# Kernel optimization log

Hardware: AMD Instinct MI355X
Metric: run time of the kernel (lower is better)

Reference implementation:

```python
import jax, jax.numpy as jnp
import numpy as np

V, E, C, H = 32000, 512, 512, 1024
B, S = 8, 512
EPS = 1e-5


def _ln(x, g, b):
    m = jnp.mean(x, axis=-1, keepdims=True)
    v = jnp.var(x, axis=-1, keepdims=True)
    return (x - m) * jax.lax.rsqrt(v + EPS) * g + b


def setup_inputs() -> dict:
    key = jax.random.key(0)
    ks = jax.random.split(key, 12)
    std = 0.02
    return {
        "input_ids": jax.random.randint(ks[0], (B, S), 0, V, dtype=jnp.int32),
        "emb": jax.random.normal(ks[1], (V, E), jnp.float32) * std,
        "emb_g": jnp.ones((E,), jnp.float32),
        "emb_b": jnp.zeros((E,), jnp.float32),
        "W1": jax.random.normal(ks[2], (E + C, H), jnp.float32) * std,
        "b1": jnp.zeros((H,), jnp.float32),
        "W2": jax.random.normal(ks[3], (H, H), jnp.float32) * std,
        "b2": jnp.zeros((H,), jnp.float32),
        "Wout": jax.random.normal(ks[4], (H, V), jnp.float32) * std,
        "bout": jnp.zeros((V,), jnp.float32),
        "Wg": jax.random.normal(ks[5], (H + C, C), jnp.float32) * std,
        "bg": jnp.zeros((C,), jnp.float32),
        "Wc": jax.random.normal(ks[6], (H + C, C), jnp.float32) * std,
        "bc": jnp.zeros((C,), jnp.float32),
        "cn_g": jnp.ones((C,), jnp.float32),
        "cn_b": jnp.zeros((C,), jnp.float32),
    }


def reference(input_ids, emb, emb_g, emb_b, W1, b1, W2, b2, Wout, bout,
              Wg, bg, Wc, bc, cn_g, cn_b):
    # token embedding + norm: [B,S,E]
    tok = _ln(emb[input_ids], emb_g, emb_b)
    tok_t = jnp.swapaxes(tok, 0, 1)  # [S,B,E] for scan over time

    def step(context, x_t):
        # context: [B,C], x_t: [B,E]
        fnn_in = jnp.concatenate([x_t, context], axis=-1)          # [B,E+C]
        h1 = jax.nn.relu(fnn_in @ W1 + b1)                          # [B,H]
        h2 = jax.nn.relu(h1 @ W2 + b2)                              # [B,H]
        logits_t = h2 @ Wout + bout                                 # [B,V]
        comb = jnp.concatenate([h2, context], axis=-1)              # [B,H+C]
        gate = jax.nn.sigmoid(comb @ Wg + bg)
        cand = jnp.tanh(comb @ Wc + bc)
        new_ctx = gate * cand + (1.0 - gate) * context
        new_ctx = jnp.clip(_ln(new_ctx, cn_g, cn_b), -10.0, 10.0)
        return new_ctx, (logits_t, new_ctx)

    ctx0 = jnp.zeros((input_ids.shape[0], C), jnp.float32)
    _, (logits, traj) = jax.lax.scan(step, ctx0, tok_t)
    logits = jnp.swapaxes(logits, 0, 1)  # [B,S,V]
    traj = jnp.swapaxes(traj, 0, 1)      # [B,S,C]
    return logits, traj
```

## Files before the change

kernel.cpp:

```cpp
#include <hip/hip_runtime.h>

typedef unsigned short u16;
typedef unsigned int u32;
typedef unsigned long long u64;
typedef __attribute__((ext_vector_type(8))) short bf16x8;
typedef __attribute__((ext_vector_type(4))) float f32x4;

#define SMEM_SCAN 147968

__device__ __forceinline__ u16 f2bf(float f) {
  u32 u = __float_as_uint(f);
  u += 0x7fffu + ((u >> 16) & 1u);
  return (u16)(u >> 16);
}

__device__ __forceinline__ void async16(const void* g, void* l) {
  __builtin_amdgcn_global_load_lds((const __attribute__((address_space(1))) void*)g,
                                   (__attribute__((address_space(3))) void*)l, 16, 0, 0);
}

__device__ __forceinline__ void st_f32(float* p, float v) {
  __hip_atomic_store(p, v, __ATOMIC_RELAXED, __HIP_MEMORY_SCOPE_AGENT);
}
__device__ __forceinline__ void st_u16(u16* p, u16 v) {
  __hip_atomic_store(p, v, __ATOMIC_RELAXED, __HIP_MEMORY_SCOPE_AGENT);
}
__device__ __forceinline__ void st_f32x2(float* p, float a, float b) {
  u64 v = ((u64)__float_as_uint(b) << 32) | (u64)__float_as_uint(a);
  __hip_atomic_store((u64*)p, v, __ATOMIC_RELAXED, __HIP_MEMORY_SCOPE_AGENT);
}
__device__ __forceinline__ u32 ld_u32(const u32* p) {
  return __hip_atomic_load(p, __ATOMIC_RELAXED, __HIP_MEMORY_SCOPE_AGENT);
}

__device__ __forceinline__ void gridbar(u32* bar, u32 target, int wg) {
  __syncthreads();
  const int tid = threadIdx.x;
  if (wg == 0) {
    if (tid < 64) {
      const u32* a0 = bar + tid;
      const u32* a1 = bar + 64 + tid;
      for (;;) {
        u32 v0 = ld_u32(a0);
        u32 v1 = ld_u32(a1);
        bool ok = ((v0 >= target) | (tid == 0)) & (v1 >= target);
        if (__all(ok)) break;
        __builtin_amdgcn_s_sleep(2);
      }
      if (tid == 0)
        __hip_atomic_store(bar + 160, target, __ATOMIC_RELAXED, __HIP_MEMORY_SCOPE_AGENT);
    }
  } else if (tid == 0) {
    __hip_atomic_store(bar + wg, target, __ATOMIC_RELAXED, __HIP_MEMORY_SCOPE_AGENT);
    while (ld_u32(bar + 160) < target)
      __builtin_amdgcn_s_sleep(2);
  }
  if (tid == 0) __builtin_amdgcn_fence(__ATOMIC_ACQUIRE, "agent");
  __syncthreads();
}

__global__ void __launch_bounds__(256)
k_embed_f32(const int* __restrict__ ids, const float* __restrict__ emb,
            const float* __restrict__ g, const float* __restrict__ b, float* __restrict__ tok) {
  int r = blockIdx.x;
  int s = r >> 3, bch = r & 7;
  int id = ids[bch * 512 + s];
  const float* row = emb + (size_t)id * 512;
  int tid = threadIdx.x;
  float2 v = *(const float2*)&row[tid * 2];
  float sum = v.x + v.y, sq = v.x * v.x + v.y * v.y;
  #pragma unroll
  for (int o = 1; o < 64; o <<= 1) { sum += __shfl_xor(sum, o); sq += __shfl_xor(sq, o); }
  __shared__ float rs[4][2];
  int w = tid >> 6;
  if ((tid & 63) == 0) { rs[w][0] = sum; rs[w][1] = sq; }
  __syncthreads();
  float S = rs[0][0] + rs[1][0] + rs[2][0] + rs[3][0];
  float Q = rs[0][1] + rs[1][1] + rs[2][1] + rs[3][1];
  float m = S * (1.f / 512.f);
  float rstd = rsqrtf(Q * (1.f / 512.f) - m * m + 1e-5f);
  int e = tid * 2;
  float2 o2;
  o2.x = (v.x - m) * rstd * g[e] + b[e];
  o2.y = (v.y - m) * rstd * g[e + 1] + b[e + 1];
  *(float2*)&tok[(size_t)r * 512 + e] = o2;
}

__global__ void __launch_bounds__(256)
k_transpose(const float* __restrict__ src, u16* __restrict__ dst,
            int K, int N, int stride) {
  __shared__ float tl[64][65];
  int k0 = blockIdx.x << 6, n0 = blockIdx.y << 6;
  int tid = threadIdx.x;
  int a = tid >> 6, c = tid & 63;
  #pragma unroll
  for (int p = 0; p < 64; p += 4)
    tl[p + a][c] = src[(size_t)(k0 + p + a) * stride + n0 + c];
  __syncthreads();
  #pragma unroll
  for (int p = 0; p < 64; p += 4)
    dst[(size_t)(n0 + p + a) * K + k0 + c] = f2bf(tl[c][p + a]);
}

__global__ void __launch_bounds__(256)
k_transpose_f32(const float* __restrict__ src, float* __restrict__ dst,
                int K, int N, int stride) {
  __shared__ float tl[64][65];
  int k0 = blockIdx.x << 6, n0 = blockIdx.y << 6;
  int tid = threadIdx.x;
  int a = tid >> 6, c = tid & 63;
  #pragma unroll
  for (int p = 0; p < 64; p += 4)
    tl[p + a][c] = src[(size_t)(k0 + p + a) * stride + n0 + c];
  __syncthreads();
  #pragma unroll
  for (int p = 0; p < 64; p += 4)
    dst[(size_t)(n0 + p + a) * K + k0 + c] = tl[c][p + a];
}

__global__ void __launch_bounds__(256)
k_gemm_f32(const float* __restrict__ A, const float* __restrict__ BT,
           const float* __restrict__ bias, float* __restrict__ C, int K, int N) {
  __shared__ float Atl[64][17];
  __shared__ float Btl[64][17];
  int tid = threadIdx.x;
  int m0 = blockIdx.x << 6, n0 = blockIdx.y << 6;
  int lr = tid >> 2, lk = (tid & 3) << 2;
  int tm = (tid >> 4) << 2, tn = (tid & 15) << 2;
  float acc[4][4] = {{0.f}};
  for (int k0 = 0; k0 < K; k0 += 16) {
    float4 av = *(const float4*)&A[(size_t)(m0 + lr) * K + k0 + lk];
    float4 bv = *(const float4*)&BT[(size_t)(n0 + lr) * K + k0 + lk];
    __syncthreads();
    Atl[lr][lk] = av.x; Atl[lr][lk + 1] = av.y; Atl[lr][lk + 2] = av.z; Atl[lr][lk + 3] = av.w;
    Btl[lr][lk] = bv.x; Btl[lr][lk + 1] = bv.y; Btl[lr][lk + 2] = bv.z; Btl[lr][lk + 3] = bv.w;
    __syncthreads();
    #pragma unroll
    for (int kk = 0; kk < 16; kk++) {
      float a0 = Atl[tm][kk], a1 = Atl[tm + 1][kk], a2 = Atl[tm + 2][kk], a3 = Atl[tm + 3][kk];
      float b0 = Btl[tn][kk], b1 = Btl[tn + 1][kk], b2 = Btl[tn + 2][kk], b3 = Btl[tn + 3][kk];
      acc[0][0] += a0 * b0; acc[0][1] += a0 * b1; acc[0][2] += a0 * b2; acc[0][3] += a0 * b3;
      acc[1][0] += a1 * b0; acc[1][1] += a1 * b1; acc[1][2] += a1 * b2; acc[1][3] += a1 * b3;
      acc[2][0] += a2 * b0; acc[2][1] += a2 * b1; acc[2][2] += a2 * b2; acc[2][3] += a2 * b3;
      acc[3][0] += a3 * b0; acc[3][1] += a3 * b1; acc[3][2] += a3 * b2; acc[3][3] += a3 * b3;
    }
  }
  #pragma unroll
  for (int a = 0; a < 4; a++)
    #pragma unroll
    for (int b = 0; b < 4; b++)
      C[(size_t)(m0 + tm + a) * N + n0 + tn + b] = acc[a][b] + bias[n0 + tn + b];
}

__global__ void __launch_bounds__(256)
k_gemm_logits(const u16* __restrict__ A, const u16* __restrict__ B,
              const float* __restrict__ bias, float* __restrict__ C, int K) {
  __shared__ u16 As[128 * 32];
  __shared__ u16 Bs[128 * 32];
  int tid = threadIdx.x;
  int w = tid >> 6, l = tid & 63;
  int m0 = blockIdx.x * 128, n0 = blockIdx.y * 128;
  const u16* pA0 = A + (size_t)(m0 + w * 32 + (l >> 2)) * K + (l & 3) * 8;
  const u16* pB0 = B + (size_t)(n0 + w * 32 + (l >> 2)) * K + (l & 3) * 8;
  u16* lA0 = As + w * 1024;
  u16* lB0 = Bs + w * 1024;

  f32x4 acc[4][4];
  #pragma unroll
  for (int i = 0; i < 4; i++)
    #pragma unroll
    for (int j = 0; j < 4; j++) { f32x4 z = {0.f, 0.f, 0.f, 0.f}; acc[i][j] = z; }

  #pragma unroll 1
  for (int k0 = 0; k0 < K; k0 += 32) {
    async16(pA0, lA0);
    async16(pA0 + 16 * K, lA0 + 512);
    async16(pB0, lB0);
    async16(pB0 + 16 * K, lB0 + 512);
    pA0 += 32; pB0 += 32;
    __syncthreads();
    bf16x8 a[4], b[4];
    #pragma unroll
    for (int i = 0; i < 4; i++)
      a[i] = *(const bf16x8*)(As + ((w & 1) * 64 + i * 16 + (l & 15)) * 32 + (l >> 4) * 8);
    #pragma unroll
    for (int j = 0; j < 4; j++)
      b[j] = *(const bf16x8*)(Bs + ((w >> 1) * 64 + j * 16 + (l & 15)) * 32 + (l >> 4) * 8);
    #pragma unroll
    for (int i = 0; i < 4; i++)
      #pragma unroll
      for (int j = 0; j < 4; j++)
        acc[i][j] = __builtin_amdgcn_mfma_f32_16x16x32_bf16(a[i], b[j], acc[i][j], 0, 0, 0);
    __syncthreads();
  }

  #pragma unroll
  for (int j = 0; j < 4; j++) {
    int gn = n0 + (w >> 1) * 64 + j * 16 + (l & 15);
    float bj = bias[gn];
    #pragma unroll
    for (int i = 0; i < 4; i++) {
      int gmB = m0 + (w & 1) * 64 + i * 16 + (l >> 4) * 4;
      #pragma unroll
      for (int e = 0; e < 4; e++) {
        int gm = gmB + e;
        C[(size_t)((gm & 7) * 512 + (gm >> 3)) * 32000 + gn] = acc[i][j][e] + bj;
      }
    }
  }
}

__global__ void __launch_bounds__(512)
k_scan(const float* __restrict__ W1cT, const float* __restrict__ W2T,
       const float* __restrict__ WgcT, const float* __restrict__ WccT,
       const float* __restrict__ WghT, const float* __restrict__ WchT,
       const float* __restrict__ b2v, const float* __restrict__ bgv,
       const float* __restrict__ bcv, const float* __restrict__ cng,
       const float* __restrict__ cnb, const float* __restrict__ pre1,
       float* __restrict__ h1f, float* __restrict__ h2f,
       float* __restrict__ pre_ctx, u16* __restrict__ h2all,
       float* __restrict__ traj, u32* __restrict__ bar) {
  extern __shared__ float smem[];
  float* w1   = smem;
  float* wgc  = w1 + 4096;
  float* w2   = wgc + 4096;
  float* wgh  = w2 + 8192;
  float* ctxn = wgh + 8192;
  float* hst  = ctxn + 4096;
  float* gcc  = hst + 8192;
  float* pscr = gcc + 64;

  const int tid = threadIdx.x;
  const int wid = blockIdx.x;
  const int g   = tid >> 5;
  const int s   = tid & 31;
  const int gg  = tid >> 6;
  const int l   = tid & 63;

  {
    const float4* srcs[6] = {
      (const float4*)(W1cT + (size_t)wid * 4096),
      (const float4*)(WgcT + (size_t)wid * 2048),
      (const float4*)(WccT + (size_t)wid * 2048),
      (const float4*)(W2T  + (size_t)wid * 8192),
      (const float4*)(WghT + (size_t)wid * 4096),
      (const float4*)(WchT + (size_t)wid * 4096)};
    float4* dsts[6] = {(float4*)w1, (float4*)wgc, (float4*)(wgc + 2048),
                       (float4*)w2, (float4*)wgh, (float4*)(wgh + 4096)};
    const int n4[6] = {1024, 512, 512, 2048, 1024, 1024};
    #pragma unroll
    for (int q = 0; q < 6; q++)
      for (int i = tid; i < n4[q]; i += 512) dsts[q][i] = srcs[q][i];
  }

  const int l8 = l * 8;
  const float4 cga = *(const float4*)&cng[l8];
  const float4 cgb = *(const float4*)&cng[l8 + 4];
  const float4 cba = *(const float4*)&cnb[l8];
  const float4 cbb = *(const float4*)&cnb[l8 + 4];
  const float b2j = b2v[(wid << 3) + gg];
  float bgj = 0.f, bcj = 0.f;
  if (tid < 32) {
    int j = (wid << 2) + (tid >> 3);
    bgj = bgv[j]; bcj = bcv[j];
  }
  __syncthreads();

  u32 ep = 0;

  #pragma unroll 1
  for (int t = 0; t < 512; ++t) {
    float pre1v = 0.f;
    if (g < 8 && s < 8)
      pre1v = pre1[(size_t)((t << 3) + s) * 1024 + (wid << 3) + g];

    if (t > 0) {
      const float* pr = pre_ctx + gg * 512 + l8;
      float4 v0 = *(const float4*)pr;
      float4 v1 = *(const float4*)(pr + 4);
      float sum = v0.x + v0.y + v0.z + v0.w + v1.x + v1.y + v1.z + v1.w;
      float sq  = v0.x*v0.x + v0.y*v0.y + v0.z*v0.z + v0.w*v0.w
                + v1.x*v1.x + v1.y*v1.y + v1.z*v1.z + v1.w*v1.w;
      #pragma unroll
      for (int o = 1; o < 64; o <<= 1) { sum += __shfl_xor(sum, o); sq += __shfl_xor(sq, o); }
      float m = sum * (1.f / 512.f);
      float rstd = rsqrtf(sq * (1.f / 512.f) - m * m + 1e-5f);
      float4 c0, c1;
      c0.x = fminf(fmaxf((v0.x - m) * rstd * cga.x + cba.x, -10.f), 10.f);
      c0.y = fminf(fmaxf((v0.y - m) * rstd * cga.y + cba.y, -10.f), 10.f);
      c0.z = fminf(fmaxf((v0.z - m) * rstd * cga.z + cba.z, -10.f), 10.f);
      c0.w = fminf(fmaxf((v0.w - m) * rstd * cga.w + cba.w, -10.f), 10.f);
      c1.x = fminf(fmaxf((v1.x - m) * rstd * cgb.x + cbb.x, -10.f), 10.f);
      c1.y = fminf(fmaxf((v1.y - m) * rstd * cgb.y + cbb.y, -10.f), 10.f);
      c1.z = fminf(fmaxf((v1.z - m) * rstd * cgb.z + cbb.z, -10.f), 10.f);
      c1.w = fminf(fmaxf((v1.w - m) * rstd * cgb.w + cbb.w, -10.f), 10.f);
      *(float4*)(ctxn + gg * 512 + l8) = c0;
      *(float4*)(ctxn + gg * 512 + l8 + 4) = c1;
      if (wid == 0) {
        float* tr = traj + (size_t)(gg * 512 + (t - 1)) * 512 + l8;
        st_f32x2(tr,     c0.x, c0.y);
        st_f32x2(tr + 2, c0.z, c0.w);
        st_f32x2(tr + 4, c1.x, c1.y);
        st_f32x2(tr + 6, c1.z, c1.w);
      }
    } else {
      float4 z = {0.f, 0.f, 0.f, 0.f};
      *(float4*)(ctxn + gg * 512 + l8) = z;
      *(float4*)(ctxn + gg * 512 + l8 + 4) = z;
    }
    __syncthreads();

    {
      const float* wsl = (g < 8) ? (w1 + g * 512) : (wgc + (g - 8) * 512);
      float acc[8] = {0.f, 0.f, 0.f, 0.f, 0.f, 0.f, 0.f, 0.f};
      #pragma unroll
      for (int i = 0; i < 4; i++) {
        int kb = (s << 2) + (i << 7);
        float4 wv = *(const float4*)(wsl + kb);
        #pragma unroll
        for (int r = 0; r < 8; r++) {
          float4 cv = *(const float4*)(ctxn + r * 512 + kb);
          acc[r] += cv.x * wv.x + cv.y * wv.y + cv.z * wv.z + cv.w * wv.w;
        }
      }
      #pragma unroll
      for (int r = 0; r < 8; r++) {
        float v = acc[r];
        v += __shfl_xor(v, 1);  v += __shfl_xor(v, 2);  v += __shfl_xor(v, 4);
        v += __shfl_xor(v, 8);  v += __shfl_xor(v, 16);
        acc[r] = v;
      }
      if (s < 8) {
        if (g < 8) st_f32(&h1f[s * 1024 + (wid << 3) + g], fmaxf(pre1v + acc[s], 0.f));
        else       gcc[(g - 8) * 8 + s] = acc[s];
      }
    }
    gridbar(bar, ++ep, wid);

    #pragma unroll
    for (int j = 0; j < 4; j++) {
      int idx = (tid + j * 512) << 2;
      *(float4*)(hst + idx) = *(const float4*)(h1f + idx);
    }
    __syncthreads();
    {
      const float* wsl = w2 + gg * 1024;
      float acc[8] = {0.f, 0.f, 0.f, 0.f, 0.f, 0.f, 0.f, 0.f};
      #pragma unroll
      for (int i = 0; i < 4; i++) {
        int kb = (l << 2) + (i << 8);
        float4 wv = *(const float4*)(wsl + kb);
        #pragma unroll
        for (int r = 0; r < 8; r++) {
          float4 hv = *(const float4*)(hst + r * 1024 + kb);
          acc[r] += hv.x * wv.x + hv.y * wv.y + hv.z * wv.z + hv.w * wv.w;
        }
      }
      #pragma unroll
      for (int r = 0; r < 8; r++) {
        float v = acc[r];
        v += __shfl_xor(v, 1);  v += __shfl_xor(v, 2);  v += __shfl_xor(v, 4);
        v += __shfl_xor(v, 8);  v += __shfl_xor(v, 16); v += __shfl_xor(v, 32);
        acc[r] = v;
      }
      if (l < 8) {
        int col = (wid << 3) + gg;
        float h = fmaxf(acc[l] + b2j, 0.f);
        st_f32(&h2f[l * 1024 + col], h);
        st_u16(&h2all[(size_t)((t << 3) + l) * 1024 + col], f2bf(h));
      }
    }
    gridbar(bar, ++ep, wid);

    #pragma unroll
    for (int j = 0; j < 4; j++) {
      int idx = (tid + j * 512) << 2;
      *(float4*)(hst + idx) = *(const float4*)(h2f + idx);
    }
    __syncthreads();
    {
      const float* wsl = wgh + gg * 1024;
      float acc[8] = {0.f, 0.f, 0.f, 0.f, 0.f, 0.f, 0.f, 0.f};
      #pragma unroll
      for (int i = 0; i < 4; i++) {
        int kb = (l << 2) + (i << 8);
        float4 wv = *(const float4*)(wsl + kb);
        #pragma unroll
        for (int r = 0; r < 8; r++) {
          float4 hv = *(const float4*)(hst + r * 1024 + kb);
          acc[r] += hv.x * wv.x + hv.y * wv.y + hv.z * wv.z + hv.w * wv.w;
        }
      }
      #pragma unroll
      for (int r = 0; r < 8; r++) {
        float v = acc[r];
        v += __shfl_xor(v, 1);  v += __shfl_xor(v, 2);  v += __shfl_xor(v, 4);
        v += __shfl_xor(v, 8);  v += __shfl_xor(v, 16); v += __shfl_xor(v, 32);
        acc[r] = v;
      }
      if (l < 8) pscr[gg * 8 + l] = acc[l];
    }
    __syncthreads();
    if (tid < 32) {
      int c = tid >> 3, r = tid & 7, j = (wid << 2) + c;
      float gd = pscr[c * 8 + r]       + gcc[c * 8 + r]       + bgj;
      float cd = pscr[(4 + c) * 8 + r] + gcc[(4 + c) * 8 + r] + bcj;
      float gate = 1.f / (1.f + __expf(-gd));
      float cand = tanhf(cd);
      st_f32(&pre_ctx[r * 512 + j], gate * cand + (1.f - gate) * ctxn[r * 512 + j]);
    }
    gridbar(bar, ++ep, wid);
  }

  if (wid == 0) {
    const float* pr = pre_ctx + gg * 512 + l8;
    float4 v0 = *(const float4*)pr;
    float4 v1 = *(const float4*)(pr + 4);
    float sum = v0.x + v0.y + v0.z + v0.w + v1.x + v1.y + v1.z + v1.w;
    float sq  = v0.x*v0.x + v0.y*v0.y + v0.z*v0.z + v0.w*v0.w
              + v1.x*v1.x + v1.y*v1.y + v1.z*v1.z + v1.w*v1.w;
    #pragma unroll
    for (int o = 1; o < 64; o <<= 1) { sum += __shfl_xor(sum, o); sq += __shfl_xor(sq, o); }
    float m = sum * (1.f / 512.f);
    float rstd = rsqrtf(sq * (1.f / 512.f) - m * m + 1e-5f);
    float4 c0, c1;
    c0.x = fminf(fmaxf((v0.x - m) * rstd * cga.x + cba.x, -10.f), 10.f);
    c0.y = fminf(fmaxf((v0.y - m) * rstd * cga.y + cba.y, -10.f), 10.f);
    c0.z = fminf(fmaxf((v0.z - m) * rstd * cga.z + cba.z, -10.f), 10.f);
    c0.w = fminf(fmaxf((v0.w - m) * rstd * cga.w + cba.w, -10.f), 10.f);
    c1.x = fminf(fmaxf((v1.x - m) * rstd * cgb.x + cbb.x, -10.f), 10.f);
    c1.y = fminf(fmaxf((v1.y - m) * rstd * cgb.y + cbb.y, -10.f), 10.f);
    c1.z = fminf(fmaxf((v1.z - m) * rstd * cgb.z + cbb.z, -10.f), 10.f);
    c1.w = fminf(fmaxf((v1.w - m) * rstd * cgb.w + cbb.w, -10.f), 10.f);
    float* tr = traj + (size_t)(gg * 512 + 511) * 512 + l8;
    *(float4*)tr = c0; *(float4*)(tr + 4) = c1;
  }
}

extern "C" void kernel_launch(void* const* d_in, const int* in_sizes, int n_in,
                              void* d_out, int out_size, void* d_ws, size_t ws_size,
                              hipStream_t stream) {
  const int*   ids  = (const int*)  d_in[0];
  const float* emb  = (const float*)d_in[1];
  const float* embg = (const float*)d_in[2];
  const float* embb = (const float*)d_in[3];
  const float* W1   = (const float*)d_in[4];
  const float* b1   = (const float*)d_in[5];
  const float* W2   = (const float*)d_in[6];
  const float* b2   = (const float*)d_in[7];
  const float* Wout = (const float*)d_in[8];
  const float* bout = (const float*)d_in[9];
  const float* Wg   = (const float*)d_in[10];
  const float* bg   = (const float*)d_in[11];
  const float* Wc   = (const float*)d_in[12];
  const float* bc   = (const float*)d_in[13];
  const float* cng  = (const float*)d_in[14];
  const float* cnb  = (const float*)d_in[15];

  float* out  = (float*)d_out;
  float* traj = out + (size_t)131072000;

  char* ws = (char*)d_ws;
  u16*   WoutT  = (u16*)(ws);
  float* tokf   = (float*)(ws + 65536000);
  float* W1xT   = (float*)(ws + 73924608);
  float* pre1   = (float*)(ws + 76021760);
  u16*   h2all  = (u16*)(ws + 92798976);
  float* W1cT   = (float*)(ws + 65536000);
  float* W2T    = (float*)(ws + 67633152);
  float* WgcT   = (float*)(ws + 71827456);
  float* WccT   = (float*)(ws + 73924608);
  float* WghT   = (float*)(ws + 101187584);
  float* WchT   = (float*)(ws + 103284736);
  float* h1f    = (float*)(ws + 105381888);
  float* h2f    = (float*)(ws + 105414656);
  float* prectx = (float*)(ws + 105447424);
  u32*   bar    = (u32*)(ws + 105463808);

  hipMemsetAsync(bar, 0, 4096, stream);

  k_transpose<<<dim3(16, 500), dim3(256), 0, stream>>>(Wout, WoutT, 1024, 32000, 32000);
  k_transpose_f32<<<dim3(8, 16), dim3(256), 0, stream>>>(W1, W1xT, 512, 1024, 1024);
  k_embed_f32<<<dim3(4096), dim3(256), 0, stream>>>(ids, emb, embg, embb, tokf);
  k_gemm_f32<<<dim3(64, 16), dim3(256), 0, stream>>>(tokf, W1xT, b1, pre1, 512, 1024);

  k_transpose_f32<<<dim3(8, 16), dim3(256), 0, stream>>>(W1 + 512 * 1024, W1cT, 512, 1024, 1024);
  k_transpose_f32<<<dim3(16, 16), dim3(256), 0, stream>>>(W2, W2T, 1024, 1024, 1024);
  k_transpose_f32<<<dim3(8, 8), dim3(256), 0, stream>>>(Wg + 1024 * 512, WgcT, 512, 512, 512);
  k_transpose_f32<<<dim3(8, 8), dim3(256), 0, stream>>>(Wc + 1024 * 512, WccT, 512, 512, 512);
  k_transpose_f32<<<dim3(16, 8), dim3(256), 0, stream>>>(Wg, WghT, 1024, 512, 512);
  k_transpose_f32<<<dim3(16, 8), dim3(256), 0, stream>>>(Wc, WchT, 1024, 512, 512);

  hipFuncSetAttribute(reinterpret_cast<const void*>(k_scan),
                      hipFuncAttributeMaxDynamicSharedMemorySize, SMEM_SCAN);
  void* args[] = {(void*)&W1cT, (void*)&W2T, (void*)&WgcT, (void*)&WccT,
                  (void*)&WghT, (void*)&WchT, (void*)&b2, (void*)&bg, (void*)&bc,
                  (void*)&cng, (void*)&cnb, (void*)&pre1, (void*)&h1f, (void*)&h2f,
                  (void*)&prectx, (void*)&h2all, (void*)&traj, (void*)&bar};
  hipLaunchCooperativeKernel((void*)k_scan, dim3(128), dim3(512), args, SMEM_SCAN, stream);

  k_gemm_logits<<<dim3(32, 250), dim3(256), 0, stream>>>(h2all, WoutT, bout, out, 1024);
}
```

Baseline: 8.691 ms.

## Replace centralized grid barrier with per-stage flag doorbells and double-buffered state

The scan kernel drops the two-hop master-gathered grid barrier. Each workgroup now posts a per-stage tag to its own slot in separate h1, h2 and ctx flag arrays, and every workgroup polls all 128 flags directly. The h1, h2 and context exchange buffers are double-buffered by step parity so a fast workgroup cannot overwrite data a slower one is still reading, and the trajectory store rotates across workgroups. The aim is to shorten each of the three per-timestep synchronisation points, at the cost of more polling traffic to the flag lines and a larger workspace.

```diff
diff --git a/kernel.cpp b/kernel.cpp
--- a/kernel.cpp
+++ b/kernel.cpp
@@ -33,29 +33,24 @@
   return __hip_atomic_load(p, __ATOMIC_RELAXED, __HIP_MEMORY_SCOPE_AGENT);
 }
 
-__device__ __forceinline__ void gridbar(u32* bar, u32 target, int wg) {
+__device__ __forceinline__ void db_post(u32* db, int wid, u32 tag) {
   __syncthreads();
+  if (threadIdx.x == 0)
+    __hip_atomic_store(db + wid, tag, __ATOMIC_RELAXED, __HIP_MEMORY_SCOPE_AGENT);
+}
+__device__ __forceinline__ void db_wait(const u32* db, u32 tag) {
   const int tid = threadIdx.x;
-  if (wg == 0) {
-    if (tid < 64) {
-      const u32* a0 = bar + tid;
-      const u32* a1 = bar + 64 + tid;
-      for (;;) {
-        u32 v0 = ld_u32(a0);
-        u32 v1 = ld_u32(a1);
-        bool ok = ((v0 >= target) | (tid == 0)) & (v1 >= target);
-        if (__all(ok)) break;
-        __builtin_amdgcn_s_sleep(2);
-      }
-      if (tid == 0)
-        __hip_atomic_store(bar + 160, target, __ATOMIC_RELAXED, __HIP_MEMORY_SCOPE_AGENT);
-    }
-  } else if (tid == 0) {
-    __hip_atomic_store(bar + wg, target, __ATOMIC_RELAXED, __HIP_MEMORY_SCOPE_AGENT);
-    while (ld_u32(bar + 160) < target)
-      __builtin_amdgcn_s_sleep(2);
-  }
-  if (tid == 0) __builtin_amdgcn_fence(__ATOMIC_ACQUIRE, "agent");
+  if (tid < 64) {
+    const u32* a0 = db + tid;
+    const u32* a1 = db + 64 + tid;
+    for (;;) {
+      u32 v0 = ld_u32(a0);
+      u32 v1 = ld_u32(a1);
+      if (__all((v0 >= tag) && (v1 >= tag))) break;
+      __builtin_amdgcn_s_sleep(4);
+    }
+    if (tid == 0) __builtin_amdgcn_fence(__ATOMIC_ACQUIRE, "agent");
+  }
   __syncthreads();
 }
 
@@ -219,7 +214,7 @@
        const float* __restrict__ cnb, const float* __restrict__ pre1,
        float* __restrict__ h1f, float* __restrict__ h2f,
        float* __restrict__ pre_ctx, u16* __restrict__ h2all,
-       float* __restrict__ traj, u32* __restrict__ bar) {
+       float* __restrict__ traj, u32* __restrict__ db) {
   extern __shared__ float smem[];
   float* w1   = smem;
   float* wgc  = w1 + 4096;
@@ -229,6 +224,10 @@
   float* hst  = ctxn + 4096;
   float* gcc  = hst + 8192;
   float* pscr = gcc + 64;
+
+  u32* db_h1  = db;
+  u32* db_h2  = db + 128;
+  u32* db_ctx = db + 256;
 
   const int tid = threadIdx.x;
   const int wid = blockIdx.x;
@@ -266,16 +265,22 @@
   }
   __syncthreads();
 
-  u32 ep = 0;
-
   #pragma unroll 1
   for (int t = 0; t < 512; ++t) {
+    const float* ctx_rd = pre_ctx + (t & 1) * 4096;
+    float*       ctx_wr = pre_ctx + ((t + 1) & 1) * 4096;
+    const float* h1_rd  = h1f + (t & 1) * 8192;
+    float*       h1_wr  = h1f + (t & 1) * 8192;
+    const float* h2_rd  = h2f + (t & 1) * 8192;
+    float*       h2_wr  = h2f + (t & 1) * 8192;
+
     float pre1v = 0.f;
     if (g < 8 && s < 8)
       pre1v = pre1[(size_t)((t << 3) + s) * 1024 + (wid << 3) + g];
 
     if (t > 0) {
-      const float* pr = pre_ctx + gg * 512 + l8;
+      db_wait(db_ctx, (u32)t);
+      const float* pr = ctx_rd + gg * 512 + l8;
       float4 v0 = *(const float4*)pr;
       float4 v1 = *(const float4*)(pr + 4);
       float sum = v0.x + v0.y + v0.z + v0.w + v1.x + v1.y + v1.z + v1.w;
@@ -296,7 +301,7 @@
       c1.w = fminf(fmaxf((v1.w - m) * rstd * cgb.w + cbb.w, -10.f), 10.f);
       *(float4*)(ctxn + gg * 512 + l8) = c0;
       *(float4*)(ctxn + gg * 512 + l8 + 4) = c1;
-      if (wid == 0) {
+      if (wid == ((t - 1) & 127)) {
         float* tr = traj + (size_t)(gg * 512 + (t - 1)) * 512 + l8;
         st_f32x2(tr,     c0.x, c0.y);
         st_f32x2(tr + 2, c0.z, c0.w);
@@ -331,16 +336,17 @@
         acc[r] = v;
       }
       if (s < 8) {
-        if (g < 8) st_f32(&h1f[s * 1024 + (wid << 3) + g], fmaxf(pre1v + acc[s], 0.f));
+        if (g < 8) st_f32(&h1_wr[s * 1024 + (wid << 3) + g], fmaxf(pre1v + acc[s], 0.f));
         else       gcc[(g - 8) * 8 + s] = acc[s];
       }
     }
-    gridbar(bar, ++ep, wid);
-
+    db_post(db_h1, wid, (u32)(t + 1));
+
+    db_wait(db_h1, (u32)(t + 1));
     #pragma unroll
     for (int j = 0; j < 4; j++) {
       int idx = (tid + j * 512) << 2;
-      *(float4*)(hst + idx) = *(const float4*)(h1f + idx);
+      *(float4*)(hst + idx) = *(const float4*)(h1_rd + idx);
     }
     __syncthreads();
     {
@@ -366,16 +372,17 @@
       if (l < 8) {
         int col = (wid << 3) + gg;
         float h = fmaxf(acc[l] + b2j, 0.f);
-        st_f32(&h2f[l * 1024 + col], h);
+        st_f32(&h2_wr[l * 1024 + col], h);
         st_u16(&h2all[(size_t)((t << 3) + l) * 1024 + col], f2bf(h));
       }
     }
-    gridbar(bar, ++ep, wid);
-
+    db_post(db_h2, wid, (u32)(t + 1));
+
+    db_wait(db_h2, (u32)(t + 1));
     #pragma unroll
     for (int j = 0; j < 4; j++) {
       int idx = (tid + j * 512) << 2;
-      *(float4*)(hst + idx) = *(const float4*)(h2f + idx);
+      *(float4*)(hst + idx) = *(const float4*)(h2_rd + idx);
     }
     __syncthreads();
     {
@@ -407,12 +414,13 @@
       float cd = pscr[(4 + c) * 8 + r] + gcc[(4 + c) * 8 + r] + bcj;
       float gate = 1.f / (1.f + __expf(-gd));
       float cand = tanhf(cd);
-      st_f32(&pre_ctx[r * 512 + j], gate * cand + (1.f - gate) * ctxn[r * 512 + j]);
-    }
-    gridbar(bar, ++ep, wid);
+      st_f32(&ctx_wr[r * 512 + j], gate * cand + (1.f - gate) * ctxn[r * 512 + j]);
+    }
+    db_post(db_ctx, wid, (u32)(t + 1));
   }
 
   if (wid == 0) {
+    db_wait(db_ctx, 512u);
     const float* pr = pre_ctx + gg * 512 + l8;
     float4 v0 = *(const float4*)pr;
     float4 v1 = *(const float4*)(pr + 4);
@@ -473,11 +481,11 @@
   float* WghT   = (float*)(ws + 101187584);
   float* WchT   = (float*)(ws + 103284736);
   float* h1f    = (float*)(ws + 105381888);
-  float* h2f    = (float*)(ws + 105414656);
-  float* prectx = (float*)(ws + 105447424);
-  u32*   bar    = (u32*)(ws + 105463808);
-
-  hipMemsetAsync(bar, 0, 4096, stream);
+  float* h2f    = (float*)(ws + 105447424);
+  float* prectx = (float*)(ws + 105512960);
+  u32*   db     = (u32*)(ws + 105545728);
+
+  hipMemsetAsync(db, 0, 4096, stream);
 
   k_transpose<<<dim3(16, 500), dim3(256), 0, stream>>>(Wout, WoutT, 1024, 32000, 32000);
   k_transpose_f32<<<dim3(8, 16), dim3(256), 0, stream>>>(W1, W1xT, 512, 1024, 1024);
@@ -496,7 +504,7 @@
   void* args[] = {(void*)&W1cT, (void*)&W2T, (void*)&WgcT, (void*)&WccT,
                   (void*)&WghT, (void*)&WchT, (void*)&b2, (void*)&bg, (void*)&bc,
                   (void*)&cng, (void*)&cnb, (void*)&pre1, (void*)&h1f, (void*)&h2f,
-                  (void*)&prectx, (void*)&h2all, (void*)&traj, (void*)&bar};
+                  (void*)&prectx, (void*)&h2all, (void*)&traj, (void*)&db};
   hipLaunchCooperativeKernel((void*)k_scan, dim3(128), dim3(512), args, SMEM_SCAN, stream);
 
   k_gemm_logits<<<dim3(32, 250), dim3(256), 0, stream>>>(h2all, WoutT, bout, out, 1024);
```

After: 10.60 ms. 1.22x slower.
